# Kernel optimization log

Measured on AMD Instinct MI355X. Metric: run time of the kernel, lower is better.

The kernel has to match this reference:

```python
import jax, jax.numpy as jnp
import numpy as np

DIM = 128
BATCH = 4096
NUM_NODES = 64


def setup_inputs() -> dict:
    key = jax.random.key(0)
    k1, k2, k3, k4, k5 = jax.random.split(key, 5)
    embs = jax.random.normal(k1, (BATCH * NUM_NODES, DIM), dtype=jnp.float32)
    # each consecutive block of num_nodes nodes belongs to one query graph
    batch_idx = jnp.repeat(jnp.arange(BATCH, dtype=jnp.int64), NUM_NODES)
    W1 = jax.random.normal(k2, (2 * DIM, DIM), dtype=jnp.float32) * (1.0 / np.sqrt(2 * DIM))
    b1 = jax.random.normal(k3, (DIM,), dtype=jnp.float32) * 0.01
    W2 = jax.random.normal(k4, (DIM, DIM), dtype=jnp.float32) * (1.0 / np.sqrt(DIM))
    b2 = jax.random.normal(k5, (DIM,), dtype=jnp.float32) * 0.01
    return {"embs": embs, "batch_idx": batch_idx, "W1": W1, "b1": b1,
            "W2": W2, "b2": b2, "batch_size": BATCH, "num_nodes": NUM_NODES,
            "num_anchors": 0}


def reference(embs, batch_idx, W1, b1, W2, b2, batch_size, num_nodes, num_anchors):
    dim = embs.shape[-1]
    # static non-target index set (num_anchors is a python int -> static)
    nt_idx = np.delete(np.arange(num_nodes), num_anchors)  # [num_nodes-1]
    embs = embs.reshape(batch_size, num_nodes, dim)
    bidx = batch_idx.reshape(batch_size, num_nodes)[:, nt_idx].reshape(-1)
    non_targets = embs[:, nt_idx]                       # [B, N-1, d]
    targets = embs[:, num_anchors:num_anchors + 1]      # [B, 1, d] -> broadcast
    targets = jnp.broadcast_to(targets, non_targets.shape)
    x = jnp.concatenate((targets, non_targets), axis=-1)  # [B, N-1, 2d]
    x = x.reshape(batch_size * (num_nodes - 1), 2 * dim)
    h = jax.nn.relu(x @ W1 + b1)
    h = jax.nn.relu(h @ W2 + b2)
    # scatter_add over batch ids
    out = jax.ops.segment_sum(h, bidx, num_segments=batch_size)  # [B, d]
    return out
```

## Files before the change

kernel.cpp:

```cpp
#include <hip/hip_runtime.h>


#define DIM   128
#define NODES 64
#define NTN   63

typedef short bf16x8 __attribute__((ext_vector_type(8)));
typedef float f32x4  __attribute__((ext_vector_type(4)));

__device__ __forceinline__ unsigned short f2bf(float f) {
    unsigned int u = __float_as_uint(f);
    u += 0x7FFFu + ((u >> 16) & 1u);
    return (unsigned short)(u >> 16);
}
__device__ __forceinline__ float bf2f(unsigned short h) {
    return __uint_as_float(((unsigned int)h) << 16);
}

__global__ void pack_wt(const float* __restrict__ W1,
                        const float* __restrict__ W2,
                        unsigned short* __restrict__ wt) {
    const int b     = blockIdx.x;
    const int layer = b >> 7;
    const int n     = b & 127;
    const int k     = threadIdx.x;
    const float* W  = layer ? W2 : (W1 + DIM * DIM);
    const float w   = W[k * DIM + n];
    const unsigned short hi = f2bf(w);
    const unsigned short lo = f2bf(w - bf2f(hi));
    unsigned short* base = wt + layer * (2 * DIM * DIM);
    base[n * DIM + k]             = hi;
    base[DIM * DIM + n * DIM + k] = lo;
}

__device__ __forceinline__ void gemm3(f32x4 acc[4][2],
                                      const unsigned short* sA_hi,
                                      const unsigned short* sA_lo,
                                      const unsigned short* __restrict__ bhi,
                                      const unsigned short* __restrict__ blo,
                                      int w, int l15, int g) {
    #pragma unroll
    for (int kk = 0; kk < 4; ++kk) {
        const int k0 = kk * 32 + g * 8;
        const bf16x8 bh0 = *(const bf16x8*)(bhi + (w * 32 + l15) * DIM + k0);
        const bf16x8 bl0 = *(const bf16x8*)(blo + (w * 32 + l15) * DIM + k0);
        const bf16x8 bh1 = *(const bf16x8*)(bhi + (w * 32 + 16 + l15) * DIM + k0);
        const bf16x8 bl1 = *(const bf16x8*)(blo + (w * 32 + 16 + l15) * DIM + k0);
        #pragma unroll
        for (int mi = 0; mi < 4; ++mi) {
            const int row = mi * 16 + l15;
            const int byt = row * 256 + ((k0 * 2) ^ ((row & 7) << 4));
            const bf16x8 ah = *(const bf16x8*)((const char*)sA_hi + byt);
            const bf16x8 al = *(const bf16x8*)((const char*)sA_lo + byt);
            acc[mi][0] = __builtin_amdgcn_mfma_f32_16x16x32_bf16(ah, bh0, acc[mi][0], 0, 0, 0);
            acc[mi][0] = __builtin_amdgcn_mfma_f32_16x16x32_bf16(ah, bl0, acc[mi][0], 0, 0, 0);
            acc[mi][0] = __builtin_amdgcn_mfma_f32_16x16x32_bf16(al, bh0, acc[mi][0], 0, 0, 0);
            acc[mi][1] = __builtin_amdgcn_mfma_f32_16x16x32_bf16(ah, bh1, acc[mi][1], 0, 0, 0);
            acc[mi][1] = __builtin_amdgcn_mfma_f32_16x16x32_bf16(ah, bl1, acc[mi][1], 0, 0, 0);
            acc[mi][1] = __builtin_amdgcn_mfma_f32_16x16x32_bf16(al, bh1, acc[mi][1], 0, 0, 0);
        }
    }
}

__global__ __launch_bounds__(256, 4)
void mlp_mfma(const float* __restrict__ embs,
              const float* __restrict__ W1,
              const float* __restrict__ b1,
              const float* __restrict__ b2,
              const unsigned short* __restrict__ wt,
              float* __restrict__ out) {
    __shared__ unsigned short sHi[64 * DIM];
    __shared__ unsigned short sLo[64 * DIM];
    __shared__ float sT[DIM];
    __shared__ float sP[256];

    const int b   = blockIdx.x;
    const int tid = threadIdx.x;
    const int w   = tid >> 6;
    const int ln  = tid & 63;
    const int l15 = ln & 15;
    const int g   = ln >> 4;
    const float* eb = embs + (size_t)b * (NODES * DIM);

    #pragma unroll
    for (int u = tid; u < 64 * 32; u += 256) {
        const int row = u >> 5;
        const int c0  = (u & 31) * 4;
        float4 v = make_float4(0.f, 0.f, 0.f, 0.f);
        if (row < NTN) v = *(const float4*)(eb + (row + 1) * DIM + c0);
        const float vf[4] = {v.x, v.y, v.z, v.w};
        unsigned int hp[2], lp[2];
        #pragma unroll
        for (int e = 0; e < 2; ++e) {
            const unsigned short h0 = f2bf(vf[2 * e]),     h1 = f2bf(vf[2 * e + 1]);
            const unsigned short q0 = f2bf(vf[2 * e]     - bf2f(h0));
            const unsigned short q1 = f2bf(vf[2 * e + 1] - bf2f(h1));
            hp[e] = (unsigned int)h0 | ((unsigned int)h1 << 16);
            lp[e] = (unsigned int)q0 | ((unsigned int)q1 << 16);
        }
        const int byt = row * 256 + ((c0 * 2) ^ ((row & 7) << 4));
        *(uint2*)((char*)sHi + byt) = make_uint2(hp[0], hp[1]);
        *(uint2*)((char*)sLo + byt) = make_uint2(lp[0], lp[1]);
    }

    {
        const int j  = tid & 127;
        const int h  = tid >> 7;
        const int kb = h * 64;
        float p = h ? 0.f : b1[j];
        #pragma unroll 4
        for (int k = 0; k < 64; ++k)
            p = fmaf(eb[kb + k], W1[(kb + k) * DIM + j], p);
        sP[tid] = p;
    }
    __syncthreads();
    if (tid < DIM) sT[tid] = sP[tid] + sP[DIM + tid];
    __syncthreads();

    const unsigned short* w1hi = wt;
    const unsigned short* w1lo = wt + DIM * DIM;
    const unsigned short* w2hi = wt + 2 * DIM * DIM;
    const unsigned short* w2lo = wt + 3 * DIM * DIM;

    f32x4 acc[4][2];
    {
        const float t0 = sT[w * 32 + l15];
        const float t1 = sT[w * 32 + 16 + l15];
        #pragma unroll
        for (int mi = 0; mi < 4; ++mi) {
            acc[mi][0] = (f32x4){t0, t0, t0, t0};
            acc[mi][1] = (f32x4){t1, t1, t1, t1};
        }
    }
    gemm3(acc, sHi, sLo, w1hi, w1lo, w, l15, g);
    __syncthreads();

    #pragma unroll
    for (int mi = 0; mi < 4; ++mi)
        #pragma unroll
        for (int nj = 0; nj < 2; ++nj)
            #pragma unroll
            for (int r = 0; r < 4; ++r) {
                const int row = mi * 16 + g * 4 + r;
                const int col = w * 32 + nj * 16 + l15;
                const float v = fmaxf(acc[mi][nj][r], 0.f);
                const unsigned short h = f2bf(v);
                const unsigned short l = f2bf(v - bf2f(h));
                const int byt = row * 256 + ((col * 2) ^ ((row & 7) << 4));
                *(unsigned short*)((char*)sHi + byt) = h;
                *(unsigned short*)((char*)sLo + byt) = l;
            }
    __syncthreads();

    {
        const float t0 = b2[w * 32 + l15];
        const float t1 = b2[w * 32 + 16 + l15];
        #pragma unroll
        for (int mi = 0; mi < 4; ++mi) {
            acc[mi][0] = (f32x4){t0, t0, t0, t0};
            acc[mi][1] = (f32x4){t1, t1, t1, t1};
        }
    }
    gemm3(acc, sHi, sLo, w2hi, w2lo, w, l15, g);

    float cs0 = 0.f, cs1 = 0.f;
    #pragma unroll
    for (int mi = 0; mi < 4; ++mi)
        #pragma unroll
        for (int r = 0; r < 4; ++r) {
            const bool pad = (mi == 3 && r == 3 && g == 3);
            const float v0 = fmaxf(acc[mi][0][r], 0.f);
            const float v1 = fmaxf(acc[mi][1][r], 0.f);
            if (!pad) { cs0 += v0; cs1 += v1; }
        }
    cs0 += __shfl_xor(cs0, 16); cs0 += __shfl_xor(cs0, 32);
    cs1 += __shfl_xor(cs1, 16); cs1 += __shfl_xor(cs1, 32);
    if (g == 0) {
        out[(size_t)b * DIM + w * 32 + l15]      = cs0;
        out[(size_t)b * DIM + w * 32 + 16 + l15] = cs1;
    }
}

extern "C" void kernel_launch(void* const* d_in, const int* in_sizes, int n_in,
                              void* d_out, int out_size, void* d_ws, size_t ws_size,
                              hipStream_t stream) {
    const float* embs = (const float*)d_in[0];
    const float* W1   = (const float*)d_in[2];
    const float* b1   = (const float*)d_in[3];
    const float* W2   = (const float*)d_in[4];
    const float* b2   = (const float*)d_in[5];
    float* out        = (float*)d_out;
    unsigned short* wt = (unsigned short*)d_ws;

    const int nb = in_sizes[0] / (NODES * DIM);

    pack_wt<<<256, 128, 0, stream>>>(W1, W2, wt);
    mlp_mfma<<<nb, 256, 0, stream>>>(embs, W1, b1, b2, wt, out);
}
```

Baseline: 273.9 us.

## Process eight graphs per persistent block with register prefetch and resident weights

Each block now loops over eight query graphs with 512 threads, so each wave owns 16 output columns instead of 32. The hi bf16 weight fragments stay in registers across graphs, and the next graph's embeddings are prefetched into registers while the current one is computed. The target-projection dot products for all eight graphs are computed up front. The aim is to amortize weight loads and hide global-load latency behind MFMA work. The costs are more registers per thread, fewer blocks (nb/8), and three barriers per graph. It also assumes the batch count divides by eight.

```diff
diff --git a/kernel.cpp b/kernel.cpp
--- a/kernel.cpp
+++ b/kernel.cpp
@@ -4,16 +4,17 @@
 #define DIM   128
 #define NODES 64
 #define NTN   63
+#define GB    8
 
 typedef short bf16x8 __attribute__((ext_vector_type(8)));
 typedef float f32x4  __attribute__((ext_vector_type(4)));
 
-__device__ __forceinline__ unsigned short f2bf(float f) {
+static __device__ __forceinline__ unsigned short f2bf(float f) {
     unsigned int u = __float_as_uint(f);
     u += 0x7FFFu + ((u >> 16) & 1u);
     return (unsigned short)(u >> 16);
 }
-__device__ __forceinline__ float bf2f(unsigned short h) {
+static __device__ __forceinline__ float bf2f(unsigned short h) {
     return __uint_as_float(((unsigned int)h) << 16);
 }
 
@@ -33,151 +34,169 @@
     base[DIM * DIM + n * DIM + k] = lo;
 }
 
-__device__ __forceinline__ void gemm3(f32x4 acc[4][2],
-                                      const unsigned short* sA_hi,
-                                      const unsigned short* sA_lo,
-                                      const unsigned short* __restrict__ bhi,
-                                      const unsigned short* __restrict__ blo,
-                                      int w, int l15, int g) {
-    #pragma unroll
-    for (int kk = 0; kk < 4; ++kk) {
-        const int k0 = kk * 32 + g * 8;
-        const bf16x8 bh0 = *(const bf16x8*)(bhi + (w * 32 + l15) * DIM + k0);
-        const bf16x8 bl0 = *(const bf16x8*)(blo + (w * 32 + l15) * DIM + k0);
-        const bf16x8 bh1 = *(const bf16x8*)(bhi + (w * 32 + 16 + l15) * DIM + k0);
-        const bf16x8 bl1 = *(const bf16x8*)(blo + (w * 32 + 16 + l15) * DIM + k0);
-        #pragma unroll
-        for (int mi = 0; mi < 4; ++mi) {
-            const int row = mi * 16 + l15;
-            const int byt = row * 256 + ((k0 * 2) ^ ((row & 7) << 4));
-            const bf16x8 ah = *(const bf16x8*)((const char*)sA_hi + byt);
-            const bf16x8 al = *(const bf16x8*)((const char*)sA_lo + byt);
-            acc[mi][0] = __builtin_amdgcn_mfma_f32_16x16x32_bf16(ah, bh0, acc[mi][0], 0, 0, 0);
-            acc[mi][0] = __builtin_amdgcn_mfma_f32_16x16x32_bf16(ah, bl0, acc[mi][0], 0, 0, 0);
-            acc[mi][0] = __builtin_amdgcn_mfma_f32_16x16x32_bf16(al, bh0, acc[mi][0], 0, 0, 0);
-            acc[mi][1] = __builtin_amdgcn_mfma_f32_16x16x32_bf16(ah, bh1, acc[mi][1], 0, 0, 0);
-            acc[mi][1] = __builtin_amdgcn_mfma_f32_16x16x32_bf16(ah, bl1, acc[mi][1], 0, 0, 0);
-            acc[mi][1] = __builtin_amdgcn_mfma_f32_16x16x32_bf16(al, bh1, acc[mi][1], 0, 0, 0);
-        }
-    }
-}
-
-__global__ __launch_bounds__(256, 4)
+__global__ __launch_bounds__(512, 4)
 void mlp_mfma(const float* __restrict__ embs,
               const float* __restrict__ W1,
               const float* __restrict__ b1,
               const float* __restrict__ b2,
               const unsigned short* __restrict__ wt,
               float* __restrict__ out) {
-    __shared__ unsigned short sHi[64 * DIM];
-    __shared__ unsigned short sLo[64 * DIM];
-    __shared__ float sT[DIM];
-    __shared__ float sP[256];
-
-    const int b   = blockIdx.x;
+    __shared__ unsigned short sA[2][NODES * DIM];
+    __shared__ unsigned short sH[2][NODES * DIM];
+    __shared__ float sT[GB][DIM];
+
     const int tid = threadIdx.x;
     const int w   = tid >> 6;
     const int ln  = tid & 63;
     const int l15 = ln & 15;
     const int g   = ln >> 4;
-    const float* eb = embs + (size_t)b * (NODES * DIM);
-
+    const int cw  = w * 16;
+    const long bg = (long)blockIdx.x * GB;
+    const float* ebase = embs + bg * (NODES * DIM);
+
+    bf16x8 bh[2][4];
     #pragma unroll
-    for (int u = tid; u < 64 * 32; u += 256) {
-        const int row = u >> 5;
-        const int c0  = (u & 31) * 4;
-        float4 v = make_float4(0.f, 0.f, 0.f, 0.f);
-        if (row < NTN) v = *(const float4*)(eb + (row + 1) * DIM + c0);
-        const float vf[4] = {v.x, v.y, v.z, v.w};
-        unsigned int hp[2], lp[2];
-        #pragma unroll
-        for (int e = 0; e < 2; ++e) {
-            const unsigned short h0 = f2bf(vf[2 * e]),     h1 = f2bf(vf[2 * e + 1]);
-            const unsigned short q0 = f2bf(vf[2 * e]     - bf2f(h0));
-            const unsigned short q1 = f2bf(vf[2 * e + 1] - bf2f(h1));
-            hp[e] = (unsigned int)h0 | ((unsigned int)h1 << 16);
-            lp[e] = (unsigned int)q0 | ((unsigned int)q1 << 16);
-        }
-        const int byt = row * 256 + ((c0 * 2) ^ ((row & 7) << 4));
-        *(uint2*)((char*)sHi + byt) = make_uint2(hp[0], hp[1]);
-        *(uint2*)((char*)sLo + byt) = make_uint2(lp[0], lp[1]);
+    for (int L = 0; L < 2; ++L)
+        #pragma unroll
+        for (int kk = 0; kk < 4; ++kk)
+            bh[L][kk] = *(const bf16x8*)(wt + L * 2 * DIM * DIM + (cw + l15) * DIM + kk * 32 + g * 8);
+
+    float4 pf0, pf1, pf2, pf3;
+    {
+        const float* e0 = ebase;
+        int Q;
+        Q = tid;        pf0 = (Q >> 5) < NTN ? *(const float4*)(e0 + ((Q >> 5) + 1) * DIM + (Q & 31) * 4) : make_float4(0.f, 0.f, 0.f, 0.f);
+        Q = tid + 512;  pf1 = (Q >> 5) < NTN ? *(const float4*)(e0 + ((Q >> 5) + 1) * DIM + (Q & 31) * 4) : make_float4(0.f, 0.f, 0.f, 0.f);
+        Q = tid + 1024; pf2 = (Q >> 5) < NTN ? *(const float4*)(e0 + ((Q >> 5) + 1) * DIM + (Q & 31) * 4) : make_float4(0.f, 0.f, 0.f, 0.f);
+        Q = tid + 1536; pf3 = (Q >> 5) < NTN ? *(const float4*)(e0 + ((Q >> 5) + 1) * DIM + (Q & 31) * 4) : make_float4(0.f, 0.f, 0.f, 0.f);
     }
 
-    {
-        const int j  = tid & 127;
-        const int h  = tid >> 7;
-        const int kb = h * 64;
-        float p = h ? 0.f : b1[j];
+    #pragma unroll
+    for (int q = 0; q < 2; ++q) {
+        const int idx = tid + q * 512;
+        const int bi  = idx >> 7;
+        const int j   = idx & 127;
+        const float* t = ebase + bi * (NODES * DIM);
+        float p = b1[j];
         #pragma unroll 4
-        for (int k = 0; k < 64; ++k)
-            p = fmaf(eb[kb + k], W1[(kb + k) * DIM + j], p);
-        sP[tid] = p;
+        for (int k = 0; k < DIM; ++k)
+            p = fmaf(t[k], W1[k * DIM + j], p);
+        sT[bi][j] = p;
     }
-    __syncthreads();
-    if (tid < DIM) sT[tid] = sP[tid] + sP[DIM + tid];
-    __syncthreads();
-
-    const unsigned short* w1hi = wt;
-    const unsigned short* w1lo = wt + DIM * DIM;
-    const unsigned short* w2hi = wt + 2 * DIM * DIM;
-    const unsigned short* w2lo = wt + 3 * DIM * DIM;
-
-    f32x4 acc[4][2];
-    {
-        const float t0 = sT[w * 32 + l15];
-        const float t1 = sT[w * 32 + 16 + l15];
-        #pragma unroll
-        for (int mi = 0; mi < 4; ++mi) {
-            acc[mi][0] = (f32x4){t0, t0, t0, t0};
-            acc[mi][1] = (f32x4){t1, t1, t1, t1};
-        }
-    }
-    gemm3(acc, sHi, sLo, w1hi, w1lo, w, l15, g);
-    __syncthreads();
-
-    #pragma unroll
-    for (int mi = 0; mi < 4; ++mi)
-        #pragma unroll
-        for (int nj = 0; nj < 2; ++nj)
+
+    const float tb2 = b2[cw + l15];
+
+    for (int i = 0; i < GB; ++i) {
+        {
+            float4 pv[4] = {pf0, pf1, pf2, pf3};
+            #pragma unroll
+            for (int qq = 0; qq < 4; ++qq) {
+                const int Q   = tid + qq * 512;
+                const int row = Q >> 5;
+                const int c0  = (Q & 31) * 4;
+                const float vf[4] = {pv[qq].x, pv[qq].y, pv[qq].z, pv[qq].w};
+                unsigned int hp[2], lp[2];
+                #pragma unroll
+                for (int e = 0; e < 2; ++e) {
+                    const unsigned short h0 = f2bf(vf[2 * e]),     h1 = f2bf(vf[2 * e + 1]);
+                    const unsigned short q0 = f2bf(vf[2 * e]     - bf2f(h0));
+                    const unsigned short q1 = f2bf(vf[2 * e + 1] - bf2f(h1));
+                    hp[e] = (unsigned int)h0 | ((unsigned int)h1 << 16);
+                    lp[e] = (unsigned int)q0 | ((unsigned int)q1 << 16);
+                }
+                const int byt = row * 256 + ((c0 * 2) ^ ((row & 7) << 4));
+                *(uint2*)((char*)sA[0] + byt) = make_uint2(hp[0], hp[1]);
+                *(uint2*)((char*)sA[1] + byt) = make_uint2(lp[0], lp[1]);
+            }
+        }
+        if (i + 1 < GB) {
+            const float* en = ebase + (i + 1) * (NODES * DIM);
+            int Q;
+            Q = tid;        pf0 = (Q >> 5) < NTN ? *(const float4*)(en + ((Q >> 5) + 1) * DIM + (Q & 31) * 4) : make_float4(0.f, 0.f, 0.f, 0.f);
+            Q = tid + 512;  pf1 = (Q >> 5) < NTN ? *(const float4*)(en + ((Q >> 5) + 1) * DIM + (Q & 31) * 4) : make_float4(0.f, 0.f, 0.f, 0.f);
+            Q = tid + 1024; pf2 = (Q >> 5) < NTN ? *(const float4*)(en + ((Q >> 5) + 1) * DIM + (Q & 31) * 4) : make_float4(0.f, 0.f, 0.f, 0.f);
+            Q = tid + 1536; pf3 = (Q >> 5) < NTN ? *(const float4*)(en + ((Q >> 5) + 1) * DIM + (Q & 31) * 4) : make_float4(0.f, 0.f, 0.f, 0.f);
+        }
+        __syncthreads();
+
+        f32x4 acc[4];
+        {
+            const float t0 = sT[i][cw + l15];
+            #pragma unroll
+            for (int mi = 0; mi < 4; ++mi) acc[mi] = (f32x4){t0, t0, t0, t0};
+        }
+        {
+            const unsigned short* wlo = wt + DIM * DIM;
+            bf16x8 bl[4];
+            #pragma unroll
+            for (int kk = 0; kk < 4; ++kk)
+                bl[kk] = *(const bf16x8*)(wlo + (cw + l15) * DIM + kk * 32 + g * 8);
+            #pragma unroll
+            for (int kk = 0; kk < 4; ++kk) {
+                const int kb = (kk * 32 + g * 8) * 2;
+                #pragma unroll
+                for (int mi = 0; mi < 4; ++mi) {
+                    const int row = mi * 16 + l15;
+                    const int byt = row * 256 + (kb ^ ((row & 7) << 4));
+                    const bf16x8 ah = *(const bf16x8*)((const char*)sA[0] + byt);
+                    const bf16x8 al = *(const bf16x8*)((const char*)sA[1] + byt);
+                    acc[mi] = __builtin_amdgcn_mfma_f32_16x16x32_bf16(ah, bh[0][kk], acc[mi], 0, 0, 0);
+                    acc[mi] = __builtin_amdgcn_mfma_f32_16x16x32_bf16(ah, bl[kk],    acc[mi], 0, 0, 0);
+                    acc[mi] = __builtin_amdgcn_mfma_f32_16x16x32_bf16(al, bh[0][kk], acc[mi], 0, 0, 0);
+                }
+            }
+        }
+        __syncthreads();
+
+        #pragma unroll
+        for (int mi = 0; mi < 4; ++mi)
             #pragma unroll
             for (int r = 0; r < 4; ++r) {
                 const int row = mi * 16 + g * 4 + r;
-                const int col = w * 32 + nj * 16 + l15;
-                const float v = fmaxf(acc[mi][nj][r], 0.f);
+                const int col = cw + l15;
+                const float v = fmaxf(acc[mi][r], 0.f);
                 const unsigned short h = f2bf(v);
                 const unsigned short l = f2bf(v - bf2f(h));
                 const int byt = row * 256 + ((col * 2) ^ ((row & 7) << 4));
-                *(unsigned short*)((char*)sHi + byt) = h;
-                *(unsigned short*)((char*)sLo + byt) = l;
-            }
-    __syncthreads();
-
-    {
-        const float t0 = b2[w * 32 + l15];
-        const float t1 = b2[w * 32 + 16 + l15];
-        #pragma unroll
-        for (int mi = 0; mi < 4; ++mi) {
-            acc[mi][0] = (f32x4){t0, t0, t0, t0};
-            acc[mi][1] = (f32x4){t1, t1, t1, t1};
-        }
-    }
-    gemm3(acc, sHi, sLo, w2hi, w2lo, w, l15, g);
-
-    float cs0 = 0.f, cs1 = 0.f;
-    #pragma unroll
-    for (int mi = 0; mi < 4; ++mi)
-        #pragma unroll
-        for (int r = 0; r < 4; ++r) {
-            const bool pad = (mi == 3 && r == 3 && g == 3);
-            const float v0 = fmaxf(acc[mi][0][r], 0.f);
-            const float v1 = fmaxf(acc[mi][1][r], 0.f);
-            if (!pad) { cs0 += v0; cs1 += v1; }
-        }
-    cs0 += __shfl_xor(cs0, 16); cs0 += __shfl_xor(cs0, 32);
-    cs1 += __shfl_xor(cs1, 16); cs1 += __shfl_xor(cs1, 32);
-    if (g == 0) {
-        out[(size_t)b * DIM + w * 32 + l15]      = cs0;
-        out[(size_t)b * DIM + w * 32 + 16 + l15] = cs1;
+                *(unsigned short*)((char*)sH[0] + byt) = h;
+                *(unsigned short*)((char*)sH[1] + byt) = l;
+            }
+        __syncthreads();
+
+        #pragma unroll
+        for (int mi = 0; mi < 4; ++mi) acc[mi] = (f32x4){tb2, tb2, tb2, tb2};
+        {
+            const unsigned short* wlo = wt + 3 * DIM * DIM;
+            bf16x8 bl[4];
+            #pragma unroll
+            for (int kk = 0; kk < 4; ++kk)
+                bl[kk] = *(const bf16x8*)(wlo + (cw + l15) * DIM + kk * 32 + g * 8);
+            #pragma unroll
+            for (int kk = 0; kk < 4; ++kk) {
+                const int kb = (kk * 32 + g * 8) * 2;
+                #pragma unroll
+                for (int mi = 0; mi < 4; ++mi) {
+                    const int row = mi * 16 + l15;
+                    const int byt = row * 256 + (kb ^ ((row & 7) << 4));
+                    const bf16x8 ah = *(const bf16x8*)((const char*)sH[0] + byt);
+                    const bf16x8 al = *(const bf16x8*)((const char*)sH[1] + byt);
+                    acc[mi] = __builtin_amdgcn_mfma_f32_16x16x32_bf16(ah, bh[1][kk], acc[mi], 0, 0, 0);
+                    acc[mi] = __builtin_amdgcn_mfma_f32_16x16x32_bf16(ah, bl[kk],    acc[mi], 0, 0, 0);
+                    acc[mi] = __builtin_amdgcn_mfma_f32_16x16x32_bf16(al, bh[1][kk], acc[mi], 0, 0, 0);
+                }
+            }
+        }
+
+        float cs = 0.f;
+        #pragma unroll
+        for (int mi = 0; mi < 4; ++mi)
+            #pragma unroll
+            for (int r = 0; r < 4; ++r)
+                if (!(mi == 3 && g == 3 && r == 3))
+                    cs += fmaxf(acc[mi][r], 0.f);
+        cs += __shfl_xor(cs, 16);
+        cs += __shfl_xor(cs, 32);
+        if (g == 0) out[(bg + i) * DIM + cw + l15] = cs;
     }
 }
 
@@ -193,7 +212,6 @@
     unsigned short* wt = (unsigned short*)d_ws;
 
     const int nb = in_sizes[0] / (NODES * DIM);
-
     pack_wt<<<256, 128, 0, stream>>>(W1, W2, wt);
-    mlp_mfma<<<nb, 256, 0, stream>>>(embs, W1, b1, b2, wt, out);
-}
+    mlp_mfma<<<nb / GB, 512, 0, stream>>>(embs, W1, b1, b2, wt, out);
+}
```

Result: slower. 282.4 us (+3.1%).

## Process four graphs per 512-thread block with 2x4 warp tiling

Applied to the files above, without the earlier changes.

Each block now handles four query graphs in sequence using eight warps, with the 64x128 tile split 2x4 across warps so each warp computes a 32x32 sub-tile. The target projection for all four graphs is computed up front, and partial row sums from the two warp rows are combined through shared memory before being written. The aim is to amortize block launch and weight-fetch overhead and to double the warps available for hiding latency. The cost is that the next graph's embedding load is serialized after each graph's compute, and there are extra barriers per graph, which reduces overlap compared with running many independent blocks.

```diff
diff --git a/kernel.cpp b/kernel.cpp
--- a/kernel.cpp
+++ b/kernel.cpp
@@ -4,16 +4,17 @@
 #define DIM   128
 #define NODES 64
 #define NTN   63
+#define GB    4
 
 typedef short bf16x8 __attribute__((ext_vector_type(8)));
 typedef float f32x4  __attribute__((ext_vector_type(4)));
 
-__device__ __forceinline__ unsigned short f2bf(float f) {
+static __device__ __forceinline__ unsigned short f2bf(float f) {
     unsigned int u = __float_as_uint(f);
     u += 0x7FFFu + ((u >> 16) & 1u);
     return (unsigned short)(u >> 16);
 }
-__device__ __forceinline__ float bf2f(unsigned short h) {
+static __device__ __forceinline__ float bf2f(unsigned short h) {
     return __uint_as_float(((unsigned int)h) << 16);
 }
 
@@ -33,151 +34,183 @@
     base[DIM * DIM + n * DIM + k] = lo;
 }
 
-__device__ __forceinline__ void gemm3(f32x4 acc[4][2],
-                                      const unsigned short* sA_hi,
-                                      const unsigned short* sA_lo,
-                                      const unsigned short* __restrict__ bhi,
-                                      const unsigned short* __restrict__ blo,
-                                      int w, int l15, int g) {
+static __device__ __forceinline__ void gemm3(f32x4 acc[2][2],
+                                             const unsigned short* s,
+                                             const unsigned short* __restrict__ bhp,
+                                             const unsigned short* __restrict__ blp,
+                                             int r0, int c0, int l15, int g) {
     #pragma unroll
     for (int kk = 0; kk < 4; ++kk) {
         const int k0 = kk * 32 + g * 8;
-        const bf16x8 bh0 = *(const bf16x8*)(bhi + (w * 32 + l15) * DIM + k0);
-        const bf16x8 bl0 = *(const bf16x8*)(blo + (w * 32 + l15) * DIM + k0);
-        const bf16x8 bh1 = *(const bf16x8*)(bhi + (w * 32 + 16 + l15) * DIM + k0);
-        const bf16x8 bl1 = *(const bf16x8*)(blo + (w * 32 + 16 + l15) * DIM + k0);
-        #pragma unroll
-        for (int mi = 0; mi < 4; ++mi) {
-            const int row = mi * 16 + l15;
+        const bf16x8 bh0 = *(const bf16x8*)(bhp + (c0 + l15) * DIM + k0);
+        const bf16x8 bl0 = *(const bf16x8*)(blp + (c0 + l15) * DIM + k0);
+        const bf16x8 bh1 = *(const bf16x8*)(bhp + (c0 + 16 + l15) * DIM + k0);
+        const bf16x8 bl1 = *(const bf16x8*)(blp + (c0 + 16 + l15) * DIM + k0);
+        #pragma unroll
+        for (int mi = 0; mi < 2; ++mi) {
+            const int row = r0 + mi * 16 + l15;
             const int byt = row * 256 + ((k0 * 2) ^ ((row & 7) << 4));
-            const bf16x8 ah = *(const bf16x8*)((const char*)sA_hi + byt);
-            const bf16x8 al = *(const bf16x8*)((const char*)sA_lo + byt);
+            const bf16x8 ah = *(const bf16x8*)((const char*)s + byt);
+            const bf16x8 al = *(const bf16x8*)((const char*)s + 16384 + byt);
             acc[mi][0] = __builtin_amdgcn_mfma_f32_16x16x32_bf16(ah, bh0, acc[mi][0], 0, 0, 0);
+            acc[mi][1] = __builtin_amdgcn_mfma_f32_16x16x32_bf16(ah, bh1, acc[mi][1], 0, 0, 0);
             acc[mi][0] = __builtin_amdgcn_mfma_f32_16x16x32_bf16(ah, bl0, acc[mi][0], 0, 0, 0);
+            acc[mi][1] = __builtin_amdgcn_mfma_f32_16x16x32_bf16(ah, bl1, acc[mi][1], 0, 0, 0);
             acc[mi][0] = __builtin_amdgcn_mfma_f32_16x16x32_bf16(al, bh0, acc[mi][0], 0, 0, 0);
-            acc[mi][1] = __builtin_amdgcn_mfma_f32_16x16x32_bf16(ah, bh1, acc[mi][1], 0, 0, 0);
-            acc[mi][1] = __builtin_amdgcn_mfma_f32_16x16x32_bf16(ah, bl1, acc[mi][1], 0, 0, 0);
             acc[mi][1] = __builtin_amdgcn_mfma_f32_16x16x32_bf16(al, bh1, acc[mi][1], 0, 0, 0);
         }
     }
 }
 
-__global__ __launch_bounds__(256, 4)
+__global__ __launch_bounds__(512, 8)
 void mlp_mfma(const float* __restrict__ embs,
               const float* __restrict__ W1,
               const float* __restrict__ b1,
               const float* __restrict__ b2,
               const unsigned short* __restrict__ wt,
               float* __restrict__ out) {
-    __shared__ unsigned short sHi[64 * DIM];
-    __shared__ unsigned short sLo[64 * DIM];
-    __shared__ float sT[DIM];
-    __shared__ float sP[256];
-
-    const int b   = blockIdx.x;
+    __shared__ unsigned short sAH[2][NODES * DIM];
+    __shared__ float sT[GB][DIM];
+    __shared__ float sR[2][DIM];
+
     const int tid = threadIdx.x;
     const int w   = tid >> 6;
     const int ln  = tid & 63;
     const int l15 = ln & 15;
     const int g   = ln >> 4;
-    const float* eb = embs + (size_t)b * (NODES * DIM);
-
-    #pragma unroll
-    for (int u = tid; u < 64 * 32; u += 256) {
-        const int row = u >> 5;
-        const int c0  = (u & 31) * 4;
-        float4 v = make_float4(0.f, 0.f, 0.f, 0.f);
-        if (row < NTN) v = *(const float4*)(eb + (row + 1) * DIM + c0);
-        const float vf[4] = {v.x, v.y, v.z, v.w};
-        unsigned int hp[2], lp[2];
-        #pragma unroll
-        for (int e = 0; e < 2; ++e) {
-            const unsigned short h0 = f2bf(vf[2 * e]),     h1 = f2bf(vf[2 * e + 1]);
-            const unsigned short q0 = f2bf(vf[2 * e]     - bf2f(h0));
-            const unsigned short q1 = f2bf(vf[2 * e + 1] - bf2f(h1));
-            hp[e] = (unsigned int)h0 | ((unsigned int)h1 << 16);
-            lp[e] = (unsigned int)q0 | ((unsigned int)q1 << 16);
-        }
-        const int byt = row * 256 + ((c0 * 2) ^ ((row & 7) << 4));
-        *(uint2*)((char*)sHi + byt) = make_uint2(hp[0], hp[1]);
-        *(uint2*)((char*)sLo + byt) = make_uint2(lp[0], lp[1]);
-    }
+    const int wc  = w & 3;
+    const int wr  = w >> 2;
+    const int c0  = wc * 32;
+    const int r0  = wr * 32;
+    const long bg = (long)blockIdx.x * GB;
+    const float* ebase = embs + bg * (NODES * DIM);
 
     {
+        const float* e0 = ebase;
+        #pragma unroll
+        for (int qq = 0; qq < 4; ++qq) {
+            const int Q   = tid + qq * 512;
+            const int row = Q >> 5;
+            const int c4  = (Q & 31) * 4;
+            float4 v = make_float4(0.f, 0.f, 0.f, 0.f);
+            if (row < NTN) v = *(const float4*)(e0 + (row + 1) * DIM + c4);
+            const float vf[4] = {v.x, v.y, v.z, v.w};
+            unsigned int hp[2], lp[2];
+            #pragma unroll
+            for (int e = 0; e < 2; ++e) {
+                const unsigned short h0 = f2bf(vf[2 * e]),     h1 = f2bf(vf[2 * e + 1]);
+                const unsigned short q0 = f2bf(vf[2 * e]     - bf2f(h0));
+                const unsigned short q1 = f2bf(vf[2 * e + 1] - bf2f(h1));
+                hp[e] = (unsigned int)h0 | ((unsigned int)h1 << 16);
+                lp[e] = (unsigned int)q0 | ((unsigned int)q1 << 16);
+            }
+            const int byt = row * 256 + ((c4 * 2) ^ ((row & 7) << 4));
+            *(uint2*)((char*)sAH[0] + byt) = make_uint2(hp[0], hp[1]);
+            *(uint2*)((char*)sAH[1] + byt) = make_uint2(lp[0], lp[1]);
+        }
+    }
+
+    {
+        const int bi = tid >> 7;
         const int j  = tid & 127;
-        const int h  = tid >> 7;
-        const int kb = h * 64;
-        float p = h ? 0.f : b1[j];
+        const float* t = ebase + bi * (NODES * DIM);
+        float p = b1[j];
         #pragma unroll 4
-        for (int k = 0; k < 64; ++k)
-            p = fmaf(eb[kb + k], W1[(kb + k) * DIM + j], p);
-        sP[tid] = p;
+        for (int k = 0; k < DIM; ++k)
+            p = fmaf(t[k], W1[k * DIM + j], p);
+        sT[bi][j] = p;
     }
     __syncthreads();
-    if (tid < DIM) sT[tid] = sP[tid] + sP[DIM + tid];
-    __syncthreads();
-
-    const unsigned short* w1hi = wt;
-    const unsigned short* w1lo = wt + DIM * DIM;
-    const unsigned short* w2hi = wt + 2 * DIM * DIM;
-    const unsigned short* w2lo = wt + 3 * DIM * DIM;
-
-    f32x4 acc[4][2];
-    {
-        const float t0 = sT[w * 32 + l15];
-        const float t1 = sT[w * 32 + 16 + l15];
-        #pragma unroll
-        for (int mi = 0; mi < 4; ++mi) {
-            acc[mi][0] = (f32x4){t0, t0, t0, t0};
-            acc[mi][1] = (f32x4){t1, t1, t1, t1};
-        }
-    }
-    gemm3(acc, sHi, sLo, w1hi, w1lo, w, l15, g);
-    __syncthreads();
-
-    #pragma unroll
-    for (int mi = 0; mi < 4; ++mi)
-        #pragma unroll
-        for (int nj = 0; nj < 2; ++nj)
+
+    for (int i = 0; i < GB; ++i) {
+        f32x4 acc[2][2];
+        {
+            const float t0 = sT[i][c0 + l15];
+            const float t1 = sT[i][c0 + 16 + l15];
+            #pragma unroll
+            for (int mi = 0; mi < 2; ++mi) {
+                acc[mi][0] = (f32x4){t0, t0, t0, t0};
+                acc[mi][1] = (f32x4){t1, t1, t1, t1};
+            }
+        }
+        gemm3(acc, sAH[0], wt, wt + DIM * DIM, r0, c0, l15, g);
+        __syncthreads();
+
+        #pragma unroll
+        for (int mi = 0; mi < 2; ++mi)
+            #pragma unroll
+            for (int nj = 0; nj < 2; ++nj)
+                #pragma unroll
+                for (int r = 0; r < 4; ++r) {
+                    const int row = r0 + mi * 16 + g * 4 + r;
+                    const int col = c0 + nj * 16 + l15;
+                    const float v = fmaxf(acc[mi][nj][r], 0.f);
+                    const unsigned short h = f2bf(v);
+                    const unsigned short l = f2bf(v - bf2f(h));
+                    const int byt = row * 256 + ((col * 2) ^ ((row & 7) << 4));
+                    *(unsigned short*)((char*)sAH[0] + byt) = h;
+                    *(unsigned short*)((char*)sAH[1] + byt) = l;
+                }
+        __syncthreads();
+
+        {
+            const float t0 = b2[c0 + l15];
+            const float t1 = b2[c0 + 16 + l15];
+            #pragma unroll
+            for (int mi = 0; mi < 2; ++mi) {
+                acc[mi][0] = (f32x4){t0, t0, t0, t0};
+                acc[mi][1] = (f32x4){t1, t1, t1, t1};
+            }
+        }
+        gemm3(acc, sAH[0], wt + 2 * DIM * DIM, wt + 3 * DIM * DIM, r0, c0, l15, g);
+
+        float cs0 = 0.f, cs1 = 0.f;
+        #pragma unroll
+        for (int mi = 0; mi < 2; ++mi)
             #pragma unroll
             for (int r = 0; r < 4; ++r) {
-                const int row = mi * 16 + g * 4 + r;
-                const int col = w * 32 + nj * 16 + l15;
-                const float v = fmaxf(acc[mi][nj][r], 0.f);
-                const unsigned short h = f2bf(v);
-                const unsigned short l = f2bf(v - bf2f(h));
-                const int byt = row * 256 + ((col * 2) ^ ((row & 7) << 4));
-                *(unsigned short*)((char*)sHi + byt) = h;
-                *(unsigned short*)((char*)sLo + byt) = l;
-            }
-    __syncthreads();
-
-    {
-        const float t0 = b2[w * 32 + l15];
-        const float t1 = b2[w * 32 + 16 + l15];
-        #pragma unroll
-        for (int mi = 0; mi < 4; ++mi) {
-            acc[mi][0] = (f32x4){t0, t0, t0, t0};
-            acc[mi][1] = (f32x4){t1, t1, t1, t1};
-        }
-    }
-    gemm3(acc, sHi, sLo, w2hi, w2lo, w, l15, g);
-
-    float cs0 = 0.f, cs1 = 0.f;
-    #pragma unroll
-    for (int mi = 0; mi < 4; ++mi)
-        #pragma unroll
-        for (int r = 0; r < 4; ++r) {
-            const bool pad = (mi == 3 && r == 3 && g == 3);
-            const float v0 = fmaxf(acc[mi][0][r], 0.f);
-            const float v1 = fmaxf(acc[mi][1][r], 0.f);
-            if (!pad) { cs0 += v0; cs1 += v1; }
-        }
-    cs0 += __shfl_xor(cs0, 16); cs0 += __shfl_xor(cs0, 32);
-    cs1 += __shfl_xor(cs1, 16); cs1 += __shfl_xor(cs1, 32);
-    if (g == 0) {
-        out[(size_t)b * DIM + w * 32 + l15]      = cs0;
-        out[(size_t)b * DIM + w * 32 + 16 + l15] = cs1;
+                if (wr == 1 && mi == 1 && g == 3 && r == 3) continue;
+                cs0 += fmaxf(acc[mi][0][r], 0.f);
+                cs1 += fmaxf(acc[mi][1][r], 0.f);
+            }
+        cs0 += __shfl_xor(cs0, 16); cs0 += __shfl_xor(cs0, 32);
+        cs1 += __shfl_xor(cs1, 16); cs1 += __shfl_xor(cs1, 32);
+        if (g == 0) {
+            sR[wr][c0 + l15]      = cs0;
+            sR[wr][c0 + 16 + l15] = cs1;
+        }
+        __syncthreads();
+
+        if (wr == 0 && g == 0) {
+            out[(bg + i) * DIM + c0 + l15]      = sR[0][c0 + l15]      + sR[1][c0 + l15];
+            out[(bg + i) * DIM + c0 + 16 + l15] = sR[0][c0 + 16 + l15] + sR[1][c0 + 16 + l15];
+        }
+
+        if (i + 1 < GB) {
+            const float* en = ebase + (i + 1) * (NODES * DIM);
+            #pragma unroll
+            for (int qq = 0; qq < 4; ++qq) {
+                const int Q   = tid + qq * 512;
+                const int row = Q >> 5;
+                const int c4  = (Q & 31) * 4;
+                float4 v = make_float4(0.f, 0.f, 0.f, 0.f);
+                if (row < NTN) v = *(const float4*)(en + (row + 1) * DIM + c4);
+                const float vf[4] = {v.x, v.y, v.z, v.w};
+                unsigned int hp[2], lp[2];
+                #pragma unroll
+                for (int e = 0; e < 2; ++e) {
+                    const unsigned short h0 = f2bf(vf[2 * e]),     h1 = f2bf(vf[2 * e + 1]);
+                    const unsigned short q0 = f2bf(vf[2 * e]     - bf2f(h0));
+                    const unsigned short q1 = f2bf(vf[2 * e + 1] - bf2f(h1));
+                    hp[e] = (unsigned int)h0 | ((unsigned int)h1 << 16);
+                    lp[e] = (unsigned int)q0 | ((unsigned int)q1 << 16);
+                }
+                const int byt = row * 256 + ((c4 * 2) ^ ((row & 7) << 4));
+                *(uint2*)((char*)sAH[0] + byt) = make_uint2(hp[0], hp[1]);
+                *(uint2*)((char*)sAH[1] + byt) = make_uint2(lp[0], lp[1]);
+            }
+        }
+        __syncthreads();
     }
 }
 
@@ -193,7 +226,6 @@
     unsigned short* wt = (unsigned short*)d_ws;
 
     const int nb = in_sizes[0] / (NODES * DIM);
-
     pack_wt<<<256, 128, 0, stream>>>(W1, W2, wt);
-    mlp_mfma<<<nb, 256, 0, stream>>>(embs, W1, b1, b2, wt, out);
-}
+    mlp_mfma<<<nb / GB, 512, 0, stream>>>(embs, W1, b1, b2, wt, out);
+}
```

New measurement: 498.3 us. +81.9%, slower.
